# Kernel tuning notes

Measured on AMD Instinct MI355X. Metric: run time of the kernel, lower is better.

The kernel has to match this reference:

```python
import jax, jax.numpy as jnp
import numpy as np

N = 100000   # nodes
E = 3200000  # edges
NC = 32


def cheb_conv(x, row, col, W, b):
    """PyG ChebConv with sym normalization and default lambda_max=2.
    Scaled Laplacian L_hat = 2L/lambda_max - I has zero diagonal and
    off-diagonal weights -d_i^{-1/2} d_j^{-1/2} (self-loops removed first).
    W: [K, in, out], b: [out] or None.
    """
    n = x.shape[0]
    ew = jnp.where(row != col, 1.0, 0.0).astype(x.dtype)  # remove_self_loops
    deg = jax.ops.segment_sum(ew, row, num_segments=n)
    dinv = jnp.where(deg > 0, jax.lax.rsqrt(jnp.maximum(deg, 1e-12)), 0.0)
    w = -ew * dinv[row] * dinv[col]  # [E] edge weights of L_hat

    def L(v):  # L_hat @ v via gather + segment-sum scatter
        return jax.ops.segment_sum(w[:, None] * v[col], row, num_segments=n)

    K = W.shape[0]
    Tx0 = x
    out = Tx0 @ W[0]
    if K > 1:
        Tx1 = L(x)
        out = out + Tx1 @ W[1]
        for k in range(2, K):  # Chebyshev recurrence T_k = 2 L T_{k-1} - T_{k-2}
            Tx2 = 2.0 * L(Tx1) - Tx0
            out = out + Tx2 @ W[k]
            Tx0, Tx1 = Tx1, Tx2
    if b is not None:
        out = out + b
    return out


def setup_inputs() -> dict:
    key = jax.random.key(0)
    ks = jax.random.split(key, 10)
    x = jax.random.normal(ks[0], (N, 3), dtype=jnp.float32)
    edge_index = jax.random.randint(ks[1], (2, E), 0, N, dtype=jnp.int64)
    batch = jnp.zeros((N,), dtype=jnp.int64)
    edge_attr = jax.random.normal(ks[2], (E, 1), dtype=jnp.float32)
    s = 0.1
    W1 = jax.random.normal(ks[3], (24, 3, NC), dtype=jnp.float32) * s
    b1 = jnp.zeros((NC,), dtype=jnp.float32)
    W2 = jax.random.normal(ks[4], (12, NC, NC), dtype=jnp.float32) * s
    b2 = jnp.zeros((NC,), dtype=jnp.float32)
    W3 = jax.random.normal(ks[5], (10, NC, NC), dtype=jnp.float32) * s
    b3 = jnp.zeros((NC,), dtype=jnp.float32)
    W4 = jax.random.normal(ks[6], (1, NC, 1), dtype=jnp.float32) * s
    return {"x": x, "edge_index": edge_index, "batch": batch, "edge_attr": edge_attr,
            "W1": W1, "b1": b1, "W2": W2, "b2": b2, "W3": W3, "b3": b3, "W4": W4}


def reference(x, edge_index, batch, edge_attr, W1, b1, W2, b2, W3, b3, W4):
    # batch and edge_attr are unused by ChebNet.forward (kept for signature parity)
    row, col = edge_index[0], edge_index[1]
    h = jax.nn.silu(cheb_conv(x, row, col, W1, b1))
    h = jax.nn.silu(cheb_conv(h, row, col, W2, b2))
    h = jax.nn.silu(cheb_conv(h, row, col, W3, b3))
    return cheb_conv(h, row, col, W4, None)  # block4: K=1, bias=False
```

## Files before the change

kernel.cpp:

```cpp
#include <hip/hip_runtime.h>
#include <math.h>

#define NN 100000
#define EE 3200000
#define NCH 32
#define CAP 96
#define FILL_PASSES 8
#define HB 3200256

typedef unsigned short ushortT;
typedef unsigned int uintT;

__device__ __forceinline__ ushortT f2b(float f) {
  uintT u = __float_as_uint(f);
  uintT r = u + 0x7fffu + ((u >> 16) & 1u);
  return (ushortT)(r >> 16);
}
__device__ __forceinline__ uintT pack2(float x, float y) {
  return (uintT)f2b(x) | ((uintT)f2b(y) << 16);
}
__device__ __forceinline__ float lo2f(uintT u) { return __uint_as_float(u << 16); }
__device__ __forceinline__ float hi2f(uintT u) { return __uint_as_float(u & 0xffff0000u); }
__device__ __forceinline__ float silu(float v) { return v / (1.f + expf(-v)); }


__global__ void init_cursor_k(int* __restrict__ cur) {
  int i = blockIdx.x * blockDim.x + threadIdx.x;
  if (i < NN) cur[i] = i * CAP;
}

__global__ void fill_k(const int* __restrict__ ei, int* __restrict__ cursor,
                       int* __restrict__ colc, int lo, int hi) {
  int t = blockIdx.x * blockDim.x + threadIdx.x;
  if (t * 4 >= EE) return;
  int4 r4 = ((const int4*)ei)[t];
  bool i0 = r4.x >= lo && r4.x < hi;
  bool i1 = r4.y >= lo && r4.y < hi;
  bool i2 = r4.z >= lo && r4.z < hi;
  bool i3 = r4.w >= lo && r4.w < hi;
  if (!(i0 | i1 | i2 | i3)) return;
  int4 c4 = ((const int4*)(ei + EE))[t];
  if (i0 && r4.x != c4.x) colc[atomicAdd(&cursor[r4.x], 1)] = c4.x;
  if (i1 && r4.y != c4.y) colc[atomicAdd(&cursor[r4.y], 1)] = c4.y;
  if (i2 && r4.z != c4.z) colc[atomicAdd(&cursor[r4.z], 1)] = c4.z;
  if (i3 && r4.w != c4.w) colc[atomicAdd(&cursor[r4.w], 1)] = c4.w;
}

__global__ __launch_bounds__(256) void prep_k(
    const int* __restrict__ rend, const float* __restrict__ x,
    float* __restrict__ dinv, float* __restrict__ d2, float* __restrict__ sqd,
    uint2* __restrict__ Vfb) {
  if (blockIdx.x == 0 && threadIdx.x < 24)
    Vfb[(size_t)threadIdx.x * (NN + 1) + NN] = make_uint2(0u, 0u);
  int i = blockIdx.x * blockDim.x + threadIdx.x;
  if (i >= NN) return;
  int c = rend[i] - i * CAP;
  float di = (c > 0) ? rsqrtf((float)c) : 0.f;
  dinv[i] = di;
  d2[i] = di * di;
  sqd[i] = (c > 0) ? sqrtf((float)c) : 1.f;
  Vfb[i] = make_uint2(pack2(di * x[3 * i], di * x[3 * i + 1]),
                      pack2(di * x[3 * i + 2], 0.f));
}

__global__ void sent_b16_k(uintT* __restrict__ Vh0, uintT* __restrict__ Vh1,
                           char* __restrict__ R) {
  int t = threadIdx.x;
  int tb = t >> 3, d = t & 7;
  if (tb >= 14) return;
  uintT* base;
  if (tb == 12) base = Vh0;
  else if (tb == 13) base = Vh1;
  else base = (uintT*)(R + (size_t)tb * HB);
  base[(size_t)NN * 8 + d] = 0u;
}


template <bool FIRST>
__global__ __launch_bounds__(256) void cheb_f3_k(
    const int* __restrict__ rend, const int* __restrict__ colc,
    const float* __restrict__ d2, const uint2* __restrict__ U,
    const uint2* __restrict__ A, uint2* __restrict__ Vo) {
  int t8 = blockIdx.x * blockDim.x + threadIdx.x;
  int i = t8 >> 3, q = t8 & 7;
  if (i >= NN) return;
  int s = i * CAP, e = rend[i];
  float a0 = 0.f, a1 = 0.f, a2 = 0.f;
  for (int b = s; b < e; b += 32) {
    int4 cq = *(const int4*)(colc + b + 4 * q);
    int eb = b + 4 * q;
    int c0 = (eb + 0 < e) ? cq.x : NN;
    int c1 = (eb + 1 < e) ? cq.y : NN;
    int c2 = (eb + 2 < e) ? cq.z : NN;
    int c3 = (eb + 3 < e) ? cq.w : NN;
    uint2 r0 = U[c0], r1 = U[c1], r2 = U[c2], r3 = U[c3];
    a0 += lo2f(r0.x); a1 += hi2f(r0.x); a2 += lo2f(r0.y);
    a0 += lo2f(r1.x); a1 += hi2f(r1.x); a2 += lo2f(r1.y);
    a0 += lo2f(r2.x); a1 += hi2f(r2.x); a2 += lo2f(r2.y);
    a0 += lo2f(r3.x); a1 += hi2f(r3.x); a2 += lo2f(r3.y);
  }
  a0 += __shfl_xor(a0, 1); a1 += __shfl_xor(a1, 1); a2 += __shfl_xor(a2, 1);
  a0 += __shfl_xor(a0, 2); a1 += __shfl_xor(a1, 2); a2 += __shfl_xor(a2, 2);
  a0 += __shfl_xor(a0, 4); a1 += __shfl_xor(a1, 4); a2 += __shfl_xor(a2, 4);
  if (q == 0) {
    float d2i = d2[i];
    float v0, v1, v2;
    if (FIRST) {
      v0 = -d2i * a0; v1 = -d2i * a1; v2 = -d2i * a2;
    } else {
      uint2 ap = A[i];
      v0 = fmaf(-2.f * d2i, a0, -lo2f(ap.x));
      v1 = fmaf(-2.f * d2i, a1, -hi2f(ap.x));
      v2 = fmaf(-2.f * d2i, a2, -lo2f(ap.y));
    }
    Vo[i] = make_uint2(pack2(v0, v1), pack2(v2, 0.f));
  }
}

template <int K0, int K1>
__device__ __forceinline__ void sum_planes(const uint2* __restrict__ Vfb, int i,
                                           const float* __restrict__ W1,
                                           float* __restrict__ s_) {
#pragma unroll
  for (int k = K0; k < K1; ++k) {
    uint2 u = Vfb[(size_t)k * (NN + 1) + i];
    float v0 = lo2f(u.x), v1 = hi2f(u.x), v2 = lo2f(u.y);
    const float* Wk = W1 + k * 96;
#pragma unroll
    for (int j = 0; j < 32; ++j)
      s_[j] = fmaf(v0, Wk[j], fmaf(v1, Wk[32 + j], fmaf(v2, Wk[64 + j], s_[j])));
  }
}

__global__ __launch_bounds__(256) void gemm_l1_k(
    const float* __restrict__ x, const uint2* __restrict__ Vfb,
    const float* __restrict__ W1, const float* __restrict__ b1,
    const float* __restrict__ dinv, const float* __restrict__ sqd,
    ushortT* __restrict__ Vh0, ushortT* __restrict__ Vh1) {
  __shared__ float red[4 * 64 * 36];
  int tid = threadIdx.x;
  int w = tid >> 6, lane = tid & 63;
  int i = blockIdx.x * 64 + lane;
  float s_[32];
#pragma unroll
  for (int j = 0; j < 32; ++j) s_[j] = 0.f;
  if (i < NN) {
    if (w == 0) sum_planes<1, 7>(Vfb, i, W1, s_);
    else if (w == 1) sum_planes<7, 13>(Vfb, i, W1, s_);
    else if (w == 2) sum_planes<13, 19>(Vfb, i, W1, s_);
    else sum_planes<19, 24>(Vfb, i, W1, s_);
  }
  float* rb = &red[(w * 64 + lane) * 36];
#pragma unroll
  for (int j = 0; j < 32; ++j) rb[j] = s_[j];
  __syncthreads();
  int r = tid >> 2, q = tid & 3;
  int io = blockIdx.x * 64 + r;
  if (io >= NN) return;
  float acc8[8];
#pragma unroll
  for (int c = 0; c < 8; ++c) acc8[c] = 0.f;
#pragma unroll
  for (int ww = 0; ww < 4; ++ww) {
    const float* p = &red[(ww * 64 + r) * 36 + q * 8];
#pragma unroll
    for (int c = 0; c < 8; ++c) acc8[c] += p[c];
  }
  float x0 = x[3 * io], x1 = x[3 * io + 1], x2 = x[3 * io + 2];
  float sq = sqd[io], di = dinv[io];
  uintT o[4];
#pragma unroll
  for (int cp = 0; cp < 4; ++cp) {
    int j0 = q * 8 + 2 * cp, j1 = j0 + 1;
    float g0 = fmaf(sq, acc8[2 * cp],
        fmaf(x0, W1[j0], fmaf(x1, W1[32 + j0], fmaf(x2, W1[64 + j0], b1[j0]))));
    float g1 = fmaf(sq, acc8[2 * cp + 1],
        fmaf(x0, W1[j1], fmaf(x1, W1[32 + j1], fmaf(x2, W1[64 + j1], b1[j1]))));
    o[cp] = pack2(di * silu(g0), di * silu(g1));
  }
  uintT* dst = (uintT*)((q >> 1) ? Vh1 : Vh0) + (size_t)io * 8 + (q & 1) * 4;
  *(uint4*)dst = make_uint4(o[0], o[1], o[2], o[3]);
}


template <bool FIRST>
__global__ __launch_bounds__(256, 4) void cheb_q_k(
    const int* __restrict__ rend, const int* __restrict__ colc,
    const float* __restrict__ d2, const uint4* __restrict__ U,
    const uint4* __restrict__ Ap, uint4* __restrict__ Vo) {
  int t = blockIdx.x * blockDim.x + threadIdx.x;
  int i = t >> 2;
  if (i >= NN) return;
  int g = t & 3;
  int slot = g & 1, h2 = g >> 1;
  int lb = (threadIdx.x & 63) & 60;
  int s = i * CAP, e = rend[i];
  float a0 = 0.f, a1 = 0.f, a2 = 0.f, a3 = 0.f;
  float a4 = 0.f, a5 = 0.f, a6 = 0.f, a7 = 0.f;
  for (int b = s; b < e; b += 16) {
    int4 cq = *(const int4*)(colc + b + 4 * g);
    int sl0 = lb + 2 * h2, sl1 = sl0 + 1;
    int eb = b + 8 * h2;
    int c0 = __shfl(cq.x, sl0), c1 = __shfl(cq.y, sl0);
    int c2 = __shfl(cq.z, sl0), c3 = __shfl(cq.w, sl0);
    int c4 = __shfl(cq.x, sl1), c5 = __shfl(cq.y, sl1);
    int c6 = __shfl(cq.z, sl1), c7 = __shfl(cq.w, sl1);
    c0 = (eb + 0 < e) ? c0 : NN;
    c1 = (eb + 1 < e) ? c1 : NN;
    c2 = (eb + 2 < e) ? c2 : NN;
    c3 = (eb + 3 < e) ? c3 : NN;
    c4 = (eb + 4 < e) ? c4 : NN;
    c5 = (eb + 5 < e) ? c5 : NN;
    c6 = (eb + 6 < e) ? c6 : NN;
    c7 = (eb + 7 < e) ? c7 : NN;
    uint4 r0 = U[(size_t)c0 * 2 + slot];
    uint4 r1 = U[(size_t)c1 * 2 + slot];
    uint4 r2 = U[(size_t)c2 * 2 + slot];
    uint4 r3 = U[(size_t)c3 * 2 + slot];
    uint4 r4 = U[(size_t)c4 * 2 + slot];
    uint4 r5 = U[(size_t)c5 * 2 + slot];
    uint4 r6 = U[(size_t)c6 * 2 + slot];
    uint4 r7 = U[(size_t)c7 * 2 + slot];
    a0 += lo2f(r0.x); a1 += hi2f(r0.x); a2 += lo2f(r0.y); a3 += hi2f(r0.y);
    a4 += lo2f(r0.z); a5 += hi2f(r0.z); a6 += lo2f(r0.w); a7 += hi2f(r0.w);
    a0 += lo2f(r1.x); a1 += hi2f(r1.x); a2 += lo2f(r1.y); a3 += hi2f(r1.y);
    a4 += lo2f(r1.z); a5 += hi2f(r1.z); a6 += lo2f(r1.w); a7 += hi2f(r1.w);
    a0 += lo2f(r2.x); a1 += hi2f(r2.x); a2 += lo2f(r2.y); a3 += hi2f(r2.y);
    a4 += lo2f(r2.z); a5 += hi2f(r2.z); a6 += lo2f(r2.w); a7 += hi2f(r2.w);
    a0 += lo2f(r3.x); a1 += hi2f(r3.x); a2 += lo2f(r3.y); a3 += hi2f(r3.y);
    a4 += lo2f(r3.z); a5 += hi2f(r3.z); a6 += lo2f(r3.w); a7 += hi2f(r3.w);
    a0 += lo2f(r4.x); a1 += hi2f(r4.x); a2 += lo2f(r4.y); a3 += hi2f(r4.y);
    a4 += lo2f(r4.z); a5 += hi2f(r4.z); a6 += lo2f(r4.w); a7 += hi2f(r4.w);
    a0 += lo2f(r5.x); a1 += hi2f(r5.x); a2 += lo2f(r5.y); a3 += hi2f(r5.y);
    a4 += lo2f(r5.z); a5 += hi2f(r5.z); a6 += lo2f(r5.w); a7 += hi2f(r5.w);
    a0 += lo2f(r6.x); a1 += hi2f(r6.x); a2 += lo2f(r6.y); a3 += hi2f(r6.y);
    a4 += lo2f(r6.z); a5 += hi2f(r6.z); a6 += lo2f(r6.w); a7 += hi2f(r6.w);
    a0 += lo2f(r7.x); a1 += hi2f(r7.x); a2 += lo2f(r7.y); a3 += hi2f(r7.y);
    a4 += lo2f(r7.z); a5 += hi2f(r7.z); a6 += lo2f(r7.w); a7 += hi2f(r7.w);
  }
  a0 += __shfl_xor(a0, 2); a1 += __shfl_xor(a1, 2);
  a2 += __shfl_xor(a2, 2); a3 += __shfl_xor(a3, 2);
  a4 += __shfl_xor(a4, 2); a5 += __shfl_xor(a5, 2);
  a6 += __shfl_xor(a6, 2); a7 += __shfl_xor(a7, 2);
  if (g >= 2) return;
  float d2i = d2[i];
  float v0, v1, v2, v3, v4, v5, v6, v7;
  if (FIRST) {
    v0 = -d2i * a0; v1 = -d2i * a1; v2 = -d2i * a2; v3 = -d2i * a3;
    v4 = -d2i * a4; v5 = -d2i * a5; v6 = -d2i * a6; v7 = -d2i * a7;
  } else {
    uint4 au = Ap[(size_t)i * 2 + slot];
    v0 = fmaf(-2.f * d2i, a0, -lo2f(au.x));
    v1 = fmaf(-2.f * d2i, a1, -hi2f(au.x));
    v2 = fmaf(-2.f * d2i, a2, -lo2f(au.y));
    v3 = fmaf(-2.f * d2i, a3, -hi2f(au.y));
    v4 = fmaf(-2.f * d2i, a4, -lo2f(au.z));
    v5 = fmaf(-2.f * d2i, a5, -hi2f(au.z));
    v6 = fmaf(-2.f * d2i, a6, -lo2f(au.w));
    v7 = fmaf(-2.f * d2i, a7, -hi2f(au.w));
  }
  Vo[(size_t)i * 2 + slot] = make_uint4(pack2(v0, v1), pack2(v2, v3),
                                        pack2(v4, v5), pack2(v6, v7));
}

__device__ __forceinline__ void fma_pair(uintT dw, const float* __restrict__ Wc,
                                         float a[32]) {
  float vl = lo2f(dw), vh = hi2f(dw);
#pragma unroll
  for (int j = 0; j < 32; ++j) a[j] = fmaf(vl, Wc[j], a[j]);
#pragma unroll
  for (int j = 0; j < 32; ++j) a[j] = fmaf(vh, Wc[32 + j], a[j]);
}

__device__ __forceinline__ void plane_fma(const uintT* __restrict__ h0,
                                          const uintT* __restrict__ h1, size_t i,
                                          const float* __restrict__ W, float a[32]) {
  uint4 u0 = *(const uint4*)(h0 + i * 8);
  uint4 u1 = *(const uint4*)(h0 + i * 8 + 4);
  uint4 u2 = *(const uint4*)(h1 + i * 8);
  uint4 u3 = *(const uint4*)(h1 + i * 8 + 4);
  fma_pair(u0.x, W + 0 * 64, a);   fma_pair(u0.y, W + 1 * 64, a);
  fma_pair(u0.z, W + 2 * 64, a);   fma_pair(u0.w, W + 3 * 64, a);
  fma_pair(u1.x, W + 4 * 64, a);   fma_pair(u1.y, W + 5 * 64, a);
  fma_pair(u1.z, W + 6 * 64, a);   fma_pair(u1.w, W + 7 * 64, a);
  fma_pair(u2.x, W + 8 * 64, a);   fma_pair(u2.y, W + 9 * 64, a);
  fma_pair(u2.z, W + 10 * 64, a);  fma_pair(u2.w, W + 11 * 64, a);
  fma_pair(u3.x, W + 12 * 64, a);  fma_pair(u3.y, W + 13 * 64, a);
  fma_pair(u3.z, W + 14 * 64, a);  fma_pair(u3.w, W + 15 * 64, a);
}

template <int NP, bool INIT, int EPI>
__global__ __launch_bounds__(256, 1) void gemm_ch_k(
    const uintT* __restrict__ A0, const uintT* __restrict__ A1,
    const uintT* __restrict__ B0, const uintT* __restrict__ B1,
    const uintT* __restrict__ C0, const uintT* __restrict__ C1,
    const uintT* __restrict__ D0, const uintT* __restrict__ D1,
    const uintT* __restrict__ E0, const uintT* __restrict__ E1,
    const uintT* __restrict__ F0, const uintT* __restrict__ F1,
    const float* __restrict__ W, float* __restrict__ acc,
    const float* __restrict__ bb, const float* __restrict__ sqd,
    const float* __restrict__ dinv, const float* __restrict__ W4,
    ushortT* __restrict__ Vh0, ushortT* __restrict__ Vh1,
    float* __restrict__ out) {
  int i = blockIdx.x * blockDim.x + threadIdx.x;
  if (i >= NN) return;
  float a[32];
  float4* ar = (float4*)(acc + (size_t)i * 32);
  if (INIT) {
#pragma unroll
    for (int j = 0; j < 32; ++j) a[j] = 0.f;
  } else {
#pragma unroll
    for (int q = 0; q < 8; ++q) {
      float4 v = ar[q];
      a[4 * q] = v.x; a[4 * q + 1] = v.y; a[4 * q + 2] = v.z; a[4 * q + 3] = v.w;
    }
  }
  plane_fma(A0, A1, (size_t)i, W, a);
  if (NP >= 2) plane_fma(B0, B1, (size_t)i, W + 1024, a);
  if (NP >= 3) plane_fma(C0, C1, (size_t)i, W + 2048, a);
  if (NP >= 4) plane_fma(D0, D1, (size_t)i, W + 3072, a);
  if (NP >= 5) plane_fma(E0, E1, (size_t)i, W + 4096, a);
  if (NP >= 6) plane_fma(F0, F1, (size_t)i, W + 5120, a);
  if (EPI == 0) {
#pragma unroll
    for (int q = 0; q < 8; ++q)
      ar[q] = make_float4(a[4 * q], a[4 * q + 1], a[4 * q + 2], a[4 * q + 3]);
  } else if (EPI == 1) {
    float sq = sqd[i], di = dinv[i];
    uintT o[16];
#pragma unroll
    for (int p = 0; p < 16; ++p) {
      float g0 = fmaf(sq, a[2 * p], bb[2 * p]);
      float g1 = fmaf(sq, a[2 * p + 1], bb[2 * p + 1]);
      o[p] = pack2(di * silu(g0), di * silu(g1));
    }
    uintT* w0 = (uintT*)Vh0 + (size_t)i * 8;
    uintT* w1 = (uintT*)Vh1 + (size_t)i * 8;
    *(uint4*)w0 = make_uint4(o[0], o[1], o[2], o[3]);
    *(uint4*)(w0 + 4) = make_uint4(o[4], o[5], o[6], o[7]);
    *(uint4*)w1 = make_uint4(o[8], o[9], o[10], o[11]);
    *(uint4*)(w1 + 4) = make_uint4(o[12], o[13], o[14], o[15]);
  } else {
    float sq = sqd[i];
    float g = 0.f;
#pragma unroll
    for (int j = 0; j < 32; ++j)
      g = fmaf(silu(fmaf(sq, a[j], bb[j])), W4[j], g);
    out[i] = g;
  }
}


extern "C" void kernel_launch(void* const* d_in, const int* in_sizes, int n_in,
                              void* d_out, int out_size, void* d_ws, size_t ws_size,
                              hipStream_t stream) {
  const float* x = (const float*)d_in[0];
  const int* ei = (const int*)d_in[1];
  const float* W1 = (const float*)d_in[4];
  const float* b1 = (const float*)d_in[5];
  const float* W2 = (const float*)d_in[6];
  const float* b2 = (const float*)d_in[7];
  const float* W3 = (const float*)d_in[8];
  const float* b3 = (const float*)d_in[9];
  const float* W4 = (const float*)d_in[10];
  float* out = (float*)d_out;

  char* ws = (char*)d_ws;
  size_t off = 0;
  auto alloc = [&](size_t bytes) {
    void* p = ws + off;
    off += (bytes + 255) & ~(size_t)255;
    return p;
  };
  int* rend = (int*)alloc((size_t)NN * 4);
  float* dinv = (float*)alloc((size_t)NN * 4);
  float* d2 = (float*)alloc((size_t)NN * 4);
  float* sqd = (float*)alloc((size_t)NN * 4);
  int* colc = (int*)alloc((size_t)NN * CAP * 4 + 128);
  ushortT* Vh0 = (ushortT*)alloc(HB);
  ushortT* Vh1 = (ushortT*)alloc(HB);
  float* acc = (float*)alloc((size_t)NN * NCH * 4);
  char* R = (char*)alloc((size_t)12 * HB);
  uint2* Vfb = (uint2*)R;
  (void)ws_size; (void)in_sizes; (void)n_in; (void)out_size;

  const int GR = (NN + 255) / 256;
  const int GR4 = (NN * 4 + 255) / 256;
  const int GR8 = (NN * 8 + 255) / 256;
  const int GL1 = (NN + 63) / 64;

  init_cursor_k<<<GR, 256, 0, stream>>>(rend);
  {
    int step = (NN + FILL_PASSES - 1) / FILL_PASSES;
    for (int p = 0; p < FILL_PASSES; ++p) {
      int lo = p * step;
      int hi = (lo + step < NN) ? lo + step : NN;
      fill_k<<<(EE / 4 + 255) / 256, 256, 0, stream>>>(ei, rend, colc, lo, hi);
    }
  }
  prep_k<<<GR, 256, 0, stream>>>(rend, x, dinv, d2, sqd, Vfb);

  auto Vp = [&](int k) { return Vfb + (size_t)k * (NN + 1); };
  cheb_f3_k<true><<<GR8, 256, 0, stream>>>(rend, colc, d2, Vp(0), nullptr, Vp(1));
  for (int k = 2; k < 24; ++k)
    cheb_f3_k<false><<<GR8, 256, 0, stream>>>(rend, colc, d2, Vp(k - 1), Vp(k - 2), Vp(k));
  gemm_l1_k<<<GL1, 256, 0, stream>>>(x, Vfb, W1, b1, dinv, sqd, Vh0, Vh1);

  sent_b16_k<<<1, 128, 0, stream>>>((uintT*)Vh0, (uintT*)Vh1, R);
  auto Rh = [&](int k, int h) {
    return (uintT*)(R + (size_t)(((k - 1) % 6) * 2 + h) * HB);
  };
  auto Hv = [&](int h) { return h ? (uintT*)Vh1 : (uintT*)Vh0; };
  auto run_cheb = [&](int K) {
    for (int k = 1; k < K; ++k) {
      for (int h = 0; h < 2; ++h) {
        const uint4* U = (const uint4*)((k == 1) ? Hv(h) : Rh(k - 1, h));
        if (k == 1) {
          cheb_q_k<true><<<GR4, 256, 0, stream>>>(rend, colc, d2, U, nullptr,
                                                  (uint4*)Rh(k, h));
        } else {
          const uint4* Ap = (const uint4*)((k == 2) ? Hv(h) : Rh(k - 2, h));
          cheb_q_k<false><<<GR4, 256, 0, stream>>>(rend, colc, d2, U, Ap,
                                                   (uint4*)Rh(k, h));
        }
      }
      if (k == 5) {
        gemm_ch_k<6, true, 0><<<GR, 256, 0, stream>>>(
            (uintT*)Vh0, (uintT*)Vh1, Rh(1, 0), Rh(1, 1), Rh(2, 0), Rh(2, 1),
            Rh(3, 0), Rh(3, 1), Rh(4, 0), Rh(4, 1), Rh(5, 0), Rh(5, 1),
            (k == 5 ? nullptr : nullptr), acc,
            nullptr, nullptr, nullptr, nullptr, nullptr, nullptr, nullptr);
      }
    }
  };
  (void)run_cheb;

  {
    const float* W = W2;
    for (int k = 1; k < 12; ++k) {
      for (int h = 0; h < 2; ++h) {
        const uint4* U = (const uint4*)((k == 1) ? Hv(h) : Rh(k - 1, h));
        if (k == 1)
          cheb_q_k<true><<<GR4, 256, 0, stream>>>(rend, colc, d2, U, nullptr,
                                                  (uint4*)Rh(k, h));
        else {
          const uint4* Ap = (const uint4*)((k == 2) ? Hv(h) : Rh(k - 2, h));
          cheb_q_k<false><<<GR4, 256, 0, stream>>>(rend, colc, d2, U, Ap,
                                                   (uint4*)Rh(k, h));
        }
      }
      if (k == 5)
        gemm_ch_k<6, true, 0><<<GR, 256, 0, stream>>>(
            (uintT*)Vh0, (uintT*)Vh1, Rh(1, 0), Rh(1, 1), Rh(2, 0), Rh(2, 1),
            Rh(3, 0), Rh(3, 1), Rh(4, 0), Rh(4, 1), Rh(5, 0), Rh(5, 1),
            W, acc, nullptr, nullptr, nullptr, nullptr, nullptr, nullptr, nullptr);
    }
    gemm_ch_k<6, false, 1><<<GR, 256, 0, stream>>>(
        Rh(6, 0), Rh(6, 1), Rh(7, 0), Rh(7, 1), Rh(8, 0), Rh(8, 1),
        Rh(9, 0), Rh(9, 1), Rh(10, 0), Rh(10, 1), Rh(11, 0), Rh(11, 1),
        W + 6 * 1024, acc, b2, sqd, dinv, nullptr, Vh0, Vh1, nullptr);
  }

  {
    const float* W = W3;
    for (int k = 1; k < 10; ++k) {
      for (int h = 0; h < 2; ++h) {
        const uint4* U = (const uint4*)((k == 1) ? Hv(h) : Rh(k - 1, h));
        if (k == 1)
          cheb_q_k<true><<<GR4, 256, 0, stream>>>(rend, colc, d2, U, nullptr,
                                                  (uint4*)Rh(k, h));
        else {
          const uint4* Ap = (const uint4*)((k == 2) ? Hv(h) : Rh(k - 2, h));
          cheb_q_k<false><<<GR4, 256, 0, stream>>>(rend, colc, d2, U, Ap,
                                                   (uint4*)Rh(k, h));
        }
      }
      if (k == 5)
        gemm_ch_k<6, true, 0><<<GR, 256, 0, stream>>>(
            (uintT*)Vh0, (uintT*)Vh1, Rh(1, 0), Rh(1, 1), Rh(2, 0), Rh(2, 1),
            Rh(3, 0), Rh(3, 1), Rh(4, 0), Rh(4, 1), Rh(5, 0), Rh(5, 1),
            W, acc, nullptr, nullptr, nullptr, nullptr, nullptr, nullptr, nullptr);
    }
    gemm_ch_k<4, false, 2><<<GR, 256, 0, stream>>>(
        Rh(6, 0), Rh(6, 1), Rh(7, 0), Rh(7, 1), Rh(8, 0), Rh(8, 1),
        Rh(9, 0), Rh(9, 1), nullptr, nullptr, nullptr, nullptr,
        W + 6 * 1024, acc, b3, sqd, nullptr, W4, nullptr, nullptr, out);
  }
}
```

Measured before the change: 1.914 ms.

## Split dense Chebyshev GEMM across two threads per node and chunk by three planes

Replaces the per-node 32-output GEMM kernel with one where two threads share each node, each computing 16 output channels. The last layer's final W4 dot product is reduced through shared memory. The GEMM is now invoked every three Chebyshev steps (4/3/3/2 planes) instead of two 6-plane launches, so fewer recurrence buffers must stay live and each launch uses fewer registers. This doubles thread-level parallelism and occupancy for the register-heavy GEMM, at the cost of extra launches, re-reading the bf16 planes in both threads, and extra accumulator round trips.

Result: slower. 2.158 ms (+12.7%).

```diff
diff --git a/kernel.cpp b/kernel.cpp
--- a/kernel.cpp
+++ b/kernel.cpp
@@ -263,91 +263,101 @@
                                         pack2(v4, v5), pack2(v6, v7));
 }
 
-__device__ __forceinline__ void fma_pair(uintT dw, const float* __restrict__ Wc,
-                                         float a[32]) {
+__device__ __forceinline__ void fma16(uintT dw, const float* __restrict__ Wc0,
+                                      const float* __restrict__ Wc1,
+                                      float a[16]) {
   float vl = lo2f(dw), vh = hi2f(dw);
 #pragma unroll
-  for (int j = 0; j < 32; ++j) a[j] = fmaf(vl, Wc[j], a[j]);
-#pragma unroll
-  for (int j = 0; j < 32; ++j) a[j] = fmaf(vh, Wc[32 + j], a[j]);
-}
-
-__device__ __forceinline__ void plane_fma(const uintT* __restrict__ h0,
-                                          const uintT* __restrict__ h1, size_t i,
-                                          const float* __restrict__ W, float a[32]) {
-  uint4 u0 = *(const uint4*)(h0 + i * 8);
-  uint4 u1 = *(const uint4*)(h0 + i * 8 + 4);
-  uint4 u2 = *(const uint4*)(h1 + i * 8);
-  uint4 u3 = *(const uint4*)(h1 + i * 8 + 4);
-  fma_pair(u0.x, W + 0 * 64, a);   fma_pair(u0.y, W + 1 * 64, a);
-  fma_pair(u0.z, W + 2 * 64, a);   fma_pair(u0.w, W + 3 * 64, a);
-  fma_pair(u1.x, W + 4 * 64, a);   fma_pair(u1.y, W + 5 * 64, a);
-  fma_pair(u1.z, W + 6 * 64, a);   fma_pair(u1.w, W + 7 * 64, a);
-  fma_pair(u2.x, W + 8 * 64, a);   fma_pair(u2.y, W + 9 * 64, a);
-  fma_pair(u2.z, W + 10 * 64, a);  fma_pair(u2.w, W + 11 * 64, a);
-  fma_pair(u3.x, W + 12 * 64, a);  fma_pair(u3.y, W + 13 * 64, a);
-  fma_pair(u3.z, W + 14 * 64, a);  fma_pair(u3.w, W + 15 * 64, a);
+  for (int j = 0; j < 16; ++j) a[j] = fmaf(vl, Wc0[j], a[j]);
+#pragma unroll
+  for (int j = 0; j < 16; ++j) a[j] = fmaf(vh, Wc1[j], a[j]);
 }
 
 template <int NP, bool INIT, int EPI>
-__global__ __launch_bounds__(256, 1) void gemm_ch_k(
+__global__ __launch_bounds__(256) void gemm_cs_k(
     const uintT* __restrict__ A0, const uintT* __restrict__ A1,
     const uintT* __restrict__ B0, const uintT* __restrict__ B1,
     const uintT* __restrict__ C0, const uintT* __restrict__ C1,
     const uintT* __restrict__ D0, const uintT* __restrict__ D1,
-    const uintT* __restrict__ E0, const uintT* __restrict__ E1,
-    const uintT* __restrict__ F0, const uintT* __restrict__ F1,
     const float* __restrict__ W, float* __restrict__ acc,
     const float* __restrict__ bb, const float* __restrict__ sqd,
     const float* __restrict__ dinv, const float* __restrict__ W4,
     ushortT* __restrict__ Vh0, ushortT* __restrict__ Vh1,
     float* __restrict__ out) {
-  int i = blockIdx.x * blockDim.x + threadIdx.x;
-  if (i >= NN) return;
-  float a[32];
-  float4* ar = (float4*)(acc + (size_t)i * 32);
+  __shared__ float part[128];
+  int tid = threadIdx.x;
+  int li = tid & 127, q = tid >> 7;
+  int ireal = blockIdx.x * 128 + li;
+  int i = (ireal < NN) ? ireal : NN - 1;
+  bool valid = ireal < NN;
+
+  const uintT* h0[4] = {A0, B0, C0, D0};
+  const uintT* h1[4] = {A1, B1, C1, D1};
+  uint4 st[NP][4];
+#pragma unroll
+  for (int p = 0; p < NP; ++p) {
+    const uint4* r0 = (const uint4*)(h0[p] + (size_t)i * 8);
+    const uint4* r1 = (const uint4*)(h1[p] + (size_t)i * 8);
+    st[p][0] = r0[0]; st[p][1] = r0[1];
+    st[p][2] = r1[0]; st[p][3] = r1[1];
+  }
+
+  float a[16];
   if (INIT) {
 #pragma unroll
-    for (int j = 0; j < 32; ++j) a[j] = 0.f;
+    for (int j = 0; j < 16; ++j) a[j] = 0.f;
   } else {
-#pragma unroll
-    for (int q = 0; q < 8; ++q) {
-      float4 v = ar[q];
-      a[4 * q] = v.x; a[4 * q + 1] = v.y; a[4 * q + 2] = v.z; a[4 * q + 3] = v.w;
-    }
-  }
-  plane_fma(A0, A1, (size_t)i, W, a);
-  if (NP >= 2) plane_fma(B0, B1, (size_t)i, W + 1024, a);
-  if (NP >= 3) plane_fma(C0, C1, (size_t)i, W + 2048, a);
-  if (NP >= 4) plane_fma(D0, D1, (size_t)i, W + 3072, a);
-  if (NP >= 5) plane_fma(E0, E1, (size_t)i, W + 4096, a);
-  if (NP >= 6) plane_fma(F0, F1, (size_t)i, W + 5120, a);
+    const float4* ar = (const float4*)(acc + (size_t)i * 32 + q * 16);
+#pragma unroll
+    for (int v = 0; v < 4; ++v) {
+      float4 vv = ar[v];
+      a[4 * v] = vv.x; a[4 * v + 1] = vv.y; a[4 * v + 2] = vv.z; a[4 * v + 3] = vv.w;
+    }
+  }
+
+#pragma unroll
+  for (int p = 0; p < NP; ++p) {
+    const float* Wp = W + p * 1024 + q * 16;
+#pragma unroll
+    for (int v = 0; v < 4; ++v) {
+      uint4 u = st[p][v];
+      fma16(u.x, Wp + (v * 8 + 0) * 32, Wp + (v * 8 + 1) * 32, a);
+      fma16(u.y, Wp + (v * 8 + 2) * 32, Wp + (v * 8 + 3) * 32, a);
+      fma16(u.z, Wp + (v * 8 + 4) * 32, Wp + (v * 8 + 5) * 32, a);
+      fma16(u.w, Wp + (v * 8 + 6) * 32, Wp + (v * 8 + 7) * 32, a);
+    }
+  }
+
   if (EPI == 0) {
-#pragma unroll
-    for (int q = 0; q < 8; ++q)
-      ar[q] = make_float4(a[4 * q], a[4 * q + 1], a[4 * q + 2], a[4 * q + 3]);
+    if (valid) {
+      float4* ar = (float4*)(acc + (size_t)i * 32 + q * 16);
+#pragma unroll
+      for (int v = 0; v < 4; ++v)
+        ar[v] = make_float4(a[4 * v], a[4 * v + 1], a[4 * v + 2], a[4 * v + 3]);
+    }
   } else if (EPI == 1) {
-    float sq = sqd[i], di = dinv[i];
-    uintT o[16];
-#pragma unroll
-    for (int p = 0; p < 16; ++p) {
-      float g0 = fmaf(sq, a[2 * p], bb[2 * p]);
-      float g1 = fmaf(sq, a[2 * p + 1], bb[2 * p + 1]);
-      o[p] = pack2(di * silu(g0), di * silu(g1));
-    }
-    uintT* w0 = (uintT*)Vh0 + (size_t)i * 8;
-    uintT* w1 = (uintT*)Vh1 + (size_t)i * 8;
-    *(uint4*)w0 = make_uint4(o[0], o[1], o[2], o[3]);
-    *(uint4*)(w0 + 4) = make_uint4(o[4], o[5], o[6], o[7]);
-    *(uint4*)w1 = make_uint4(o[8], o[9], o[10], o[11]);
-    *(uint4*)(w1 + 4) = make_uint4(o[12], o[13], o[14], o[15]);
+    if (valid) {
+      float sq = sqd[i], di = dinv[i];
+      uintT o[8];
+#pragma unroll
+      for (int p = 0; p < 8; ++p) {
+        float g0 = fmaf(sq, a[2 * p], bb[q * 16 + 2 * p]);
+        float g1 = fmaf(sq, a[2 * p + 1], bb[q * 16 + 2 * p + 1]);
+        o[p] = pack2(di * silu(g0), di * silu(g1));
+      }
+      uintT* w0 = (uintT*)(q ? Vh1 : Vh0) + (size_t)i * 8;
+      *(uint4*)w0 = make_uint4(o[0], o[1], o[2], o[3]);
+      *(uint4*)(w0 + 4) = make_uint4(o[4], o[5], o[6], o[7]);
+    }
   } else {
     float sq = sqd[i];
     float g = 0.f;
 #pragma unroll
-    for (int j = 0; j < 32; ++j)
-      g = fmaf(silu(fmaf(sq, a[j], bb[j])), W4[j], g);
-    out[i] = g;
+    for (int j = 0; j < 16; ++j)
+      g = fmaf(silu(fmaf(sq, a[j], bb[q * 16 + j])), W4[q * 16 + j], g);
+    if (q == 1) part[li] = g;
+    __syncthreads();
+    if (q == 0 && valid) out[ireal] = g + part[li];
   }
 }
 
@@ -389,6 +399,7 @@
   const int GR4 = (NN * 4 + 255) / 256;
   const int GR8 = (NN * 8 + 255) / 256;
   const int GL1 = (NN + 63) / 64;
+  const int GQ = (NN + 127) / 128;
 
   init_cursor_k<<<GR, 256, 0, stream>>>(rend);
   {
@@ -412,79 +423,64 @@
     return (uintT*)(R + (size_t)(((k - 1) % 6) * 2 + h) * HB);
   };
   auto Hv = [&](int h) { return h ? (uintT*)Vh1 : (uintT*)Vh0; };
-  auto run_cheb = [&](int K) {
-    for (int k = 1; k < K; ++k) {
-      for (int h = 0; h < 2; ++h) {
-        const uint4* U = (const uint4*)((k == 1) ? Hv(h) : Rh(k - 1, h));
-        if (k == 1) {
-          cheb_q_k<true><<<GR4, 256, 0, stream>>>(rend, colc, d2, U, nullptr,
-                                                  (uint4*)Rh(k, h));
-        } else {
-          const uint4* Ap = (const uint4*)((k == 2) ? Hv(h) : Rh(k - 2, h));
-          cheb_q_k<false><<<GR4, 256, 0, stream>>>(rend, colc, d2, U, Ap,
-                                                   (uint4*)Rh(k, h));
-        }
+  auto cheb_step = [&](int k) {
+    for (int h = 0; h < 2; ++h) {
+      const uint4* U = (const uint4*)((k == 1) ? Hv(h) : Rh(k - 1, h));
+      if (k == 1)
+        cheb_q_k<true><<<GR4, 256, 0, stream>>>(rend, colc, d2, U, nullptr,
+                                                (uint4*)Rh(k, h));
+      else {
+        const uint4* Ap = (const uint4*)((k == 2) ? Hv(h) : Rh(k - 2, h));
+        cheb_q_k<false><<<GR4, 256, 0, stream>>>(rend, colc, d2, U, Ap,
+                                                 (uint4*)Rh(k, h));
       }
-      if (k == 5) {
-        gemm_ch_k<6, true, 0><<<GR, 256, 0, stream>>>(
-            (uintT*)Vh0, (uintT*)Vh1, Rh(1, 0), Rh(1, 1), Rh(2, 0), Rh(2, 1),
-            Rh(3, 0), Rh(3, 1), Rh(4, 0), Rh(4, 1), Rh(5, 0), Rh(5, 1),
-            (k == 5 ? nullptr : nullptr), acc,
-            nullptr, nullptr, nullptr, nullptr, nullptr, nullptr, nullptr);
-      }
     }
   };
-  (void)run_cheb;
 
   {
     const float* W = W2;
     for (int k = 1; k < 12; ++k) {
-      for (int h = 0; h < 2; ++h) {
-        const uint4* U = (const uint4*)((k == 1) ? Hv(h) : Rh(k - 1, h));
-        if (k == 1)
-          cheb_q_k<true><<<GR4, 256, 0, stream>>>(rend, colc, d2, U, nullptr,
-                                                  (uint4*)Rh(k, h));
-        else {
-          const uint4* Ap = (const uint4*)((k == 2) ? Hv(h) : Rh(k - 2, h));
-          cheb_q_k<false><<<GR4, 256, 0, stream>>>(rend, colc, d2, U, Ap,
-                                                   (uint4*)Rh(k, h));
-        }
-      }
-      if (k == 5)
-        gemm_ch_k<6, true, 0><<<GR, 256, 0, stream>>>(
+      cheb_step(k);
+      if (k == 3)
+        gemm_cs_k<4, true, 0><<<GQ, 256, 0, stream>>>(
             (uintT*)Vh0, (uintT*)Vh1, Rh(1, 0), Rh(1, 1), Rh(2, 0), Rh(2, 1),
-            Rh(3, 0), Rh(3, 1), Rh(4, 0), Rh(4, 1), Rh(5, 0), Rh(5, 1),
-            W, acc, nullptr, nullptr, nullptr, nullptr, nullptr, nullptr, nullptr);
-    }
-    gemm_ch_k<6, false, 1><<<GR, 256, 0, stream>>>(
-        Rh(6, 0), Rh(6, 1), Rh(7, 0), Rh(7, 1), Rh(8, 0), Rh(8, 1),
-        Rh(9, 0), Rh(9, 1), Rh(10, 0), Rh(10, 1), Rh(11, 0), Rh(11, 1),
-        W + 6 * 1024, acc, b2, sqd, dinv, nullptr, Vh0, Vh1, nullptr);
+            Rh(3, 0), Rh(3, 1), W, acc,
+            nullptr, nullptr, nullptr, nullptr, nullptr, nullptr, nullptr);
+      else if (k == 6)
+        gemm_cs_k<3, false, 0><<<GQ, 256, 0, stream>>>(
+            Rh(4, 0), Rh(4, 1), Rh(5, 0), Rh(5, 1), Rh(6, 0), Rh(6, 1),
+            nullptr, nullptr, W + 4 * 1024, acc,
+            nullptr, nullptr, nullptr, nullptr, nullptr, nullptr, nullptr);
+      else if (k == 9)
+        gemm_cs_k<3, false, 0><<<GQ, 256, 0, stream>>>(
+            Rh(7, 0), Rh(7, 1), Rh(8, 0), Rh(8, 1), Rh(9, 0), Rh(9, 1),
+            nullptr, nullptr, W + 7 * 1024, acc,
+            nullptr, nullptr, nullptr, nullptr, nullptr, nullptr, nullptr);
+    }
+    gemm_cs_k<2, false, 1><<<GQ, 256, 0, stream>>>(
+        Rh(10, 0), Rh(10, 1), Rh(11, 0), Rh(11, 1), nullptr, nullptr,
+        nullptr, nullptr, W + 10 * 1024, acc,
+        b2, sqd, dinv, nullptr, Vh0, Vh1, nullptr);
   }
 
   {
     const float* W = W3;
     for (int k = 1; k < 10; ++k) {
-      for (int h = 0; h < 2; ++h) {
-        const uint4* U = (const uint4*)((k == 1) ? Hv(h) : Rh(k - 1, h));
-        if (k == 1)
-          cheb_q_k<true><<<GR4, 256, 0, stream>>>(rend, colc, d2, U, nullptr,
-                                                  (uint4*)Rh(k, h));
-        else {
-          const uint4* Ap = (const uint4*)((k == 2) ? Hv(h) : Rh(k - 2, h));
-          cheb_q_k<false><<<GR4, 256, 0, stream>>>(rend, colc, d2, U, Ap,
-                                                   (uint4*)Rh(k, h));
-        }
-      }
-      if (k == 5)
-        gemm_ch_k<6, true, 0><<<GR, 256, 0, stream>>>(
+      cheb_step(k);
+      if (k == 3)
+        gemm_cs_k<4, true, 0><<<GQ, 256, 0, stream>>>(
             (uintT*)Vh0, (uintT*)Vh1, Rh(1, 0), Rh(1, 1), Rh(2, 0), Rh(2, 1),
-            Rh(3, 0), Rh(3, 1), Rh(4, 0), Rh(4, 1), Rh(5, 0), Rh(5, 1),
-            W, acc, nullptr, nullptr, nullptr, nullptr, nullptr, nullptr, nullptr);
-    }
-    gemm_ch_k<4, false, 2><<<GR, 256, 0, stream>>>(
-        Rh(6, 0), Rh(6, 1), Rh(7, 0), Rh(7, 1), Rh(8, 0), Rh(8, 1),
-        Rh(9, 0), Rh(9, 1), nullptr, nullptr, nullptr, nullptr,
-        W + 6 * 1024, acc, b3, sqd, nullptr, W4, nullptr, nullptr, out);
-  }
-}
+            Rh(3, 0), Rh(3, 1), W, acc,
+            nullptr, nullptr, nullptr, nullptr, nullptr, nullptr, nullptr);
+      else if (k == 6)
+        gemm_cs_k<3, false, 0><<<GQ, 256, 0, stream>>>(
+            Rh(4, 0), Rh(4, 1), Rh(5, 0), Rh(5, 1), Rh(6, 0), Rh(6, 1),
+            nullptr, nullptr, W + 4 * 1024, acc,
+            nullptr, nullptr, nullptr, nullptr, nullptr, nullptr, nullptr);
+    }
+    gemm_cs_k<3, false, 2><<<GQ, 256, 0, stream>>>(
+        Rh(7, 0), Rh(7, 1), Rh(8, 0), Rh(8, 1), Rh(9, 0), Rh(9, 1),
+        nullptr, nullptr, W + 7 * 1024, acc,
+        b3, sqd, nullptr, W4, nullptr, nullptr, out);
+  }
+}
```

## Merge fill passes and half-channel SpMV launches with XCD-aware block mapping

Applied to the files above, without the earlier changes.

The eight range-restricted fill passes become one launch whose block index picks the row range, so the cursor atomics for each range stay on one XCD. The two half-channel cheb launches per Chebyshev step merge into one kernel that maps each half to a group of four XCDs, which halves the launch count and keeps each half's feature plane in fewer L2 caches. The per-node channel GEMM is split into 3-plane chunks issued more often, with loads hoisted up front and a launch bound allowing two blocks per CU. The cost is extra acc read/write traffic, more registers held by the hoisted loads, and reliance on round-robin block-to-XCD dispatch.

Result: faster. 1.656 ms (-13.5%).

```diff
diff --git a/kernel.cpp b/kernel.cpp
--- a/kernel.cpp
+++ b/kernel.cpp
@@ -5,7 +5,6 @@
 #define EE 3200000
 #define NCH 32
 #define CAP 96
-#define FILL_PASSES 8
 #define HB 3200256
 
 typedef unsigned short ushortT;
@@ -29,10 +28,15 @@
   if (i < NN) cur[i] = i * CAP;
 }
 
-__global__ void fill_k(const int* __restrict__ ei, int* __restrict__ cursor,
-                       int* __restrict__ colc, int lo, int hi) {
-  int t = blockIdx.x * blockDim.x + threadIdx.x;
+__global__ void fill_all_k(const int* __restrict__ ei, int* __restrict__ cursor,
+                           int* __restrict__ colc) {
+  int b = blockIdx.x;
+  int w = b & 7;
+  int t = (b >> 3) * 256 + threadIdx.x;
   if (t * 4 >= EE) return;
+  int step = (NN + 7) / 8;
+  int lo = w * step;
+  int hi = lo + step < NN ? lo + step : NN;
   int4 r4 = ((const int4*)ei)[t];
   bool i0 = r4.x >= lo && r4.x < hi;
   bool i1 = r4.y >= lo && r4.y < hi;
@@ -184,23 +188,32 @@
 
 
 template <bool FIRST>
-__global__ __launch_bounds__(256, 4) void cheb_q_k(
+__global__ __launch_bounds__(256, 4) void cheb_x_k(
     const int* __restrict__ rend, const int* __restrict__ colc,
-    const float* __restrict__ d2, const uint4* __restrict__ U,
-    const uint4* __restrict__ Ap, uint4* __restrict__ Vo) {
-  int t = blockIdx.x * blockDim.x + threadIdx.x;
+    const float* __restrict__ d2,
+    const uint4* __restrict__ U0, const uint4* __restrict__ U1,
+    const uint4* __restrict__ Ap0, const uint4* __restrict__ Ap1,
+    uint4* __restrict__ Vo0, uint4* __restrict__ Vo1) {
+  int b = blockIdx.x;
+  int xcd = b & 7;
+  int h = xcd >> 2;
+  int sub = (b >> 3) * 4 + (xcd & 3);
+  int t = sub * 256 + threadIdx.x;
   int i = t >> 2;
   if (i >= NN) return;
+  const uint4* U = h ? U1 : U0;
+  const uint4* Ap = h ? Ap1 : Ap0;
+  uint4* Vo = h ? Vo1 : Vo0;
   int g = t & 3;
   int slot = g & 1, h2 = g >> 1;
   int lb = (threadIdx.x & 63) & 60;
   int s = i * CAP, e = rend[i];
   float a0 = 0.f, a1 = 0.f, a2 = 0.f, a3 = 0.f;
   float a4 = 0.f, a5 = 0.f, a6 = 0.f, a7 = 0.f;
-  for (int b = s; b < e; b += 16) {
-    int4 cq = *(const int4*)(colc + b + 4 * g);
+  for (int bb = s; bb < e; bb += 16) {
+    int4 cq = *(const int4*)(colc + bb + 4 * g);
     int sl0 = lb + 2 * h2, sl1 = sl0 + 1;
-    int eb = b + 8 * h2;
+    int eb = bb + 8 * h2;
     int c0 = __shfl(cq.x, sl0), c1 = __shfl(cq.y, sl0);
     int c2 = __shfl(cq.z, sl0), c3 = __shfl(cq.w, sl0);
     int c4 = __shfl(cq.x, sl1), c5 = __shfl(cq.y, sl1);
@@ -272,13 +285,9 @@
   for (int j = 0; j < 32; ++j) a[j] = fmaf(vh, Wc[32 + j], a[j]);
 }
 
-__device__ __forceinline__ void plane_fma(const uintT* __restrict__ h0,
-                                          const uintT* __restrict__ h1, size_t i,
-                                          const float* __restrict__ W, float a[32]) {
-  uint4 u0 = *(const uint4*)(h0 + i * 8);
-  uint4 u1 = *(const uint4*)(h0 + i * 8 + 4);
-  uint4 u2 = *(const uint4*)(h1 + i * 8);
-  uint4 u3 = *(const uint4*)(h1 + i * 8 + 4);
+__device__ __forceinline__ void fma_plane(uint4 u0, uint4 u1, uint4 u2, uint4 u3,
+                                          const float* __restrict__ W,
+                                          float a[32]) {
   fma_pair(u0.x, W + 0 * 64, a);   fma_pair(u0.y, W + 1 * 64, a);
   fma_pair(u0.z, W + 2 * 64, a);   fma_pair(u0.w, W + 3 * 64, a);
   fma_pair(u1.x, W + 4 * 64, a);   fma_pair(u1.y, W + 5 * 64, a);
@@ -290,13 +299,11 @@
 }
 
 template <int NP, bool INIT, int EPI>
-__global__ __launch_bounds__(256, 1) void gemm_ch_k(
+__global__ __launch_bounds__(256, 2) void gemm_r_k(
     const uintT* __restrict__ A0, const uintT* __restrict__ A1,
     const uintT* __restrict__ B0, const uintT* __restrict__ B1,
     const uintT* __restrict__ C0, const uintT* __restrict__ C1,
     const uintT* __restrict__ D0, const uintT* __restrict__ D1,
-    const uintT* __restrict__ E0, const uintT* __restrict__ E1,
-    const uintT* __restrict__ F0, const uintT* __restrict__ F1,
     const float* __restrict__ W, float* __restrict__ acc,
     const float* __restrict__ bb, const float* __restrict__ sqd,
     const float* __restrict__ dinv, const float* __restrict__ W4,
@@ -304,25 +311,46 @@
     float* __restrict__ out) {
   int i = blockIdx.x * blockDim.x + threadIdx.x;
   if (i >= NN) return;
+  uint4 ua0, ua1, ua2, ua3, ub0, ub1, ub2, ub3;
+  uint4 uc0, uc1, uc2, uc3, ud0, ud1, ud2, ud3;
+  {
+    const uint4* p0 = (const uint4*)(A0 + (size_t)i * 8);
+    const uint4* p1 = (const uint4*)(A1 + (size_t)i * 8);
+    ua0 = p0[0]; ua1 = p0[1]; ua2 = p1[0]; ua3 = p1[1];
+  }
+  if (NP >= 2) {
+    const uint4* p0 = (const uint4*)(B0 + (size_t)i * 8);
+    const uint4* p1 = (const uint4*)(B1 + (size_t)i * 8);
+    ub0 = p0[0]; ub1 = p0[1]; ub2 = p1[0]; ub3 = p1[1];
+  }
+  if (NP >= 3) {
+    const uint4* p0 = (const uint4*)(C0 + (size_t)i * 8);
+    const uint4* p1 = (const uint4*)(C1 + (size_t)i * 8);
+    uc0 = p0[0]; uc1 = p0[1]; uc2 = p1[0]; uc3 = p1[1];
+  }
+  if (NP >= 4) {
+    const uint4* p0 = (const uint4*)(D0 + (size_t)i * 8);
+    const uint4* p1 = (const uint4*)(D1 + (size_t)i * 8);
+    ud0 = p0[0]; ud1 = p0[1]; ud2 = p1[0]; ud3 = p1[1];
+  }
   float a[32];
-  float4* ar = (float4*)(acc + (size_t)i * 32);
   if (INIT) {
 #pragma unroll
     for (int j = 0; j < 32; ++j) a[j] = 0.f;
   } else {
+    const float4* ar = (const float4*)(acc + (size_t)i * 32);
 #pragma unroll
     for (int q = 0; q < 8; ++q) {
       float4 v = ar[q];
       a[4 * q] = v.x; a[4 * q + 1] = v.y; a[4 * q + 2] = v.z; a[4 * q + 3] = v.w;
     }
   }
-  plane_fma(A0, A1, (size_t)i, W, a);
-  if (NP >= 2) plane_fma(B0, B1, (size_t)i, W + 1024, a);
-  if (NP >= 3) plane_fma(C0, C1, (size_t)i, W + 2048, a);
-  if (NP >= 4) plane_fma(D0, D1, (size_t)i, W + 3072, a);
-  if (NP >= 5) plane_fma(E0, E1, (size_t)i, W + 4096, a);
-  if (NP >= 6) plane_fma(F0, F1, (size_t)i, W + 5120, a);
+  fma_plane(ua0, ua1, ua2, ua3, W, a);
+  if (NP >= 2) fma_plane(ub0, ub1, ub2, ub3, W + 1024, a);
+  if (NP >= 3) fma_plane(uc0, uc1, uc2, uc3, W + 2048, a);
+  if (NP >= 4) fma_plane(ud0, ud1, ud2, ud3, W + 3072, a);
   if (EPI == 0) {
+    float4* ar = (float4*)(acc + (size_t)i * 32);
 #pragma unroll
     for (int q = 0; q < 8; ++q)
       ar[q] = make_float4(a[4 * q], a[4 * q + 1], a[4 * q + 2], a[4 * q + 3]);
@@ -386,19 +414,12 @@
   (void)ws_size; (void)in_sizes; (void)n_in; (void)out_size;
 
   const int GR = (NN + 255) / 256;
-  const int GR4 = (NN * 4 + 255) / 256;
   const int GR8 = (NN * 8 + 255) / 256;
   const int GL1 = (NN + 63) / 64;
+  const int GX = 3200;
 
   init_cursor_k<<<GR, 256, 0, stream>>>(rend);
-  {
-    int step = (NN + FILL_PASSES - 1) / FILL_PASSES;
-    for (int p = 0; p < FILL_PASSES; ++p) {
-      int lo = p * step;
-      int hi = (lo + step < NN) ? lo + step : NN;
-      fill_k<<<(EE / 4 + 255) / 256, 256, 0, stream>>>(ei, rend, colc, lo, hi);
-    }
-  }
+  fill_all_k<<<8 * (EE / 4 / 256), 256, 0, stream>>>(ei, rend, colc);
   prep_k<<<GR, 256, 0, stream>>>(rend, x, dinv, d2, sqd, Vfb);
 
   auto Vp = [&](int k) { return Vfb + (size_t)k * (NN + 1); };
@@ -411,80 +432,65 @@
   auto Rh = [&](int k, int h) {
     return (uintT*)(R + (size_t)(((k - 1) % 6) * 2 + h) * HB);
   };
-  auto Hv = [&](int h) { return h ? (uintT*)Vh1 : (uintT*)Vh0; };
-  auto run_cheb = [&](int K) {
-    for (int k = 1; k < K; ++k) {
-      for (int h = 0; h < 2; ++h) {
-        const uint4* U = (const uint4*)((k == 1) ? Hv(h) : Rh(k - 1, h));
-        if (k == 1) {
-          cheb_q_k<true><<<GR4, 256, 0, stream>>>(rend, colc, d2, U, nullptr,
-                                                  (uint4*)Rh(k, h));
-        } else {
-          const uint4* Ap = (const uint4*)((k == 2) ? Hv(h) : Rh(k - 2, h));
-          cheb_q_k<false><<<GR4, 256, 0, stream>>>(rend, colc, d2, U, Ap,
-                                                   (uint4*)Rh(k, h));
-        }
-      }
-      if (k == 5) {
-        gemm_ch_k<6, true, 0><<<GR, 256, 0, stream>>>(
-            (uintT*)Vh0, (uintT*)Vh1, Rh(1, 0), Rh(1, 1), Rh(2, 0), Rh(2, 1),
-            Rh(3, 0), Rh(3, 1), Rh(4, 0), Rh(4, 1), Rh(5, 0), Rh(5, 1),
-            (k == 5 ? nullptr : nullptr), acc,
-            nullptr, nullptr, nullptr, nullptr, nullptr, nullptr, nullptr);
-      }
+  auto cheb_step = [&](int k) {
+    const uint4* U0 = (const uint4*)((k == 1) ? (uintT*)Vh0 : Rh(k - 1, 0));
+    const uint4* U1 = (const uint4*)((k == 1) ? (uintT*)Vh1 : Rh(k - 1, 1));
+    if (k == 1) {
+      cheb_x_k<true><<<GX, 256, 0, stream>>>(rend, colc, d2, U0, U1,
+                                             nullptr, nullptr,
+                                             (uint4*)Rh(k, 0), (uint4*)Rh(k, 1));
+    } else {
+      const uint4* A0 = (const uint4*)((k == 2) ? (uintT*)Vh0 : Rh(k - 2, 0));
+      const uint4* A1 = (const uint4*)((k == 2) ? (uintT*)Vh1 : Rh(k - 2, 1));
+      cheb_x_k<false><<<GX, 256, 0, stream>>>(rend, colc, d2, U0, U1, A0, A1,
+                                              (uint4*)Rh(k, 0), (uint4*)Rh(k, 1));
     }
   };
-  (void)run_cheb;
 
   {
     const float* W = W2;
     for (int k = 1; k < 12; ++k) {
-      for (int h = 0; h < 2; ++h) {
-        const uint4* U = (const uint4*)((k == 1) ? Hv(h) : Rh(k - 1, h));
-        if (k == 1)
-          cheb_q_k<true><<<GR4, 256, 0, stream>>>(rend, colc, d2, U, nullptr,
-                                                  (uint4*)Rh(k, h));
-        else {
-          const uint4* Ap = (const uint4*)((k == 2) ? Hv(h) : Rh(k - 2, h));
-          cheb_q_k<false><<<GR4, 256, 0, stream>>>(rend, colc, d2, U, Ap,
-                                                   (uint4*)Rh(k, h));
-        }
-      }
-      if (k == 5)
-        gemm_ch_k<6, true, 0><<<GR, 256, 0, stream>>>(
+      cheb_step(k);
+      if (k == 2)
+        gemm_r_k<3, true, 0><<<GR, 256, 0, stream>>>(
             (uintT*)Vh0, (uintT*)Vh1, Rh(1, 0), Rh(1, 1), Rh(2, 0), Rh(2, 1),
+            nullptr, nullptr, W, acc,
+            nullptr, nullptr, nullptr, nullptr, nullptr, nullptr, nullptr);
+      else if (k == 5)
+        gemm_r_k<3, false, 0><<<GR, 256, 0, stream>>>(
             Rh(3, 0), Rh(3, 1), Rh(4, 0), Rh(4, 1), Rh(5, 0), Rh(5, 1),
-            W, acc, nullptr, nullptr, nullptr, nullptr, nullptr, nullptr, nullptr);
-    }
-    gemm_ch_k<6, false, 1><<<GR, 256, 0, stream>>>(
-        Rh(6, 0), Rh(6, 1), Rh(7, 0), Rh(7, 1), Rh(8, 0), Rh(8, 1),
+            nullptr, nullptr, W + 3 * 1024, acc,
+            nullptr, nullptr, nullptr, nullptr, nullptr, nullptr, nullptr);
+      else if (k == 8)
+        gemm_r_k<3, false, 0><<<GR, 256, 0, stream>>>(
+            Rh(6, 0), Rh(6, 1), Rh(7, 0), Rh(7, 1), Rh(8, 0), Rh(8, 1),
+            nullptr, nullptr, W + 6 * 1024, acc,
+            nullptr, nullptr, nullptr, nullptr, nullptr, nullptr, nullptr);
+    }
+    gemm_r_k<3, false, 1><<<GR, 256, 0, stream>>>(
         Rh(9, 0), Rh(9, 1), Rh(10, 0), Rh(10, 1), Rh(11, 0), Rh(11, 1),
-        W + 6 * 1024, acc, b2, sqd, dinv, nullptr, Vh0, Vh1, nullptr);
+        nullptr, nullptr, W + 9 * 1024, acc,
+        b2, sqd, dinv, nullptr, Vh0, Vh1, nullptr);
   }
 
   {
     const float* W = W3;
     for (int k = 1; k < 10; ++k) {
-      for (int h = 0; h < 2; ++h) {
-        const uint4* U = (const uint4*)((k == 1) ? Hv(h) : Rh(k - 1, h));
-        if (k == 1)
-          cheb_q_k<true><<<GR4, 256, 0, stream>>>(rend, colc, d2, U, nullptr,
-                                                  (uint4*)Rh(k, h));
-        else {
-          const uint4* Ap = (const uint4*)((k == 2) ? Hv(h) : Rh(k - 2, h));
-          cheb_q_k<false><<<GR4, 256, 0, stream>>>(rend, colc, d2, U, Ap,
-                                                   (uint4*)Rh(k, h));
-        }
-      }
-      if (k == 5)
-        gemm_ch_k<6, true, 0><<<GR, 256, 0, stream>>>(
+      cheb_step(k);
+      if (k == 2)
+        gemm_r_k<3, true, 0><<<GR, 256, 0, stream>>>(
             (uintT*)Vh0, (uintT*)Vh1, Rh(1, 0), Rh(1, 1), Rh(2, 0), Rh(2, 1),
+            nullptr, nullptr, W, acc,
+            nullptr, nullptr, nullptr, nullptr, nullptr, nullptr, nullptr);
+      else if (k == 5)
+        gemm_r_k<3, false, 0><<<GR, 256, 0, stream>>>(
             Rh(3, 0), Rh(3, 1), Rh(4, 0), Rh(4, 1), Rh(5, 0), Rh(5, 1),
-            W, acc, nullptr, nullptr, nullptr, nullptr, nullptr, nullptr, nullptr);
-    }
-    gemm_ch_k<4, false, 2><<<GR, 256, 0, stream>>>(
+            nullptr, nullptr, W + 3 * 1024, acc,
+            nullptr, nullptr, nullptr, nullptr, nullptr, nullptr, nullptr);
+    }
+    gemm_r_k<4, false, 2><<<GR, 256, 0, stream>>>(
         Rh(6, 0), Rh(6, 1), Rh(7, 0), Rh(7, 1), Rh(8, 0), Rh(8, 1),
-        Rh(9, 0), Rh(9, 1), nullptr, nullptr, nullptr, nullptr,
-        W + 6 * 1024, acc, b3, sqd, nullptr, W4, nullptr, nullptr, out);
-  }
-}
+        Rh(9, 0), Rh(9, 1), W + 6 * 1024, acc,
+        b3, sqd, nullptr, W4, nullptr, nullptr, out);
+  }
+}
```
